# Performance work log

Hardware: AMD Instinct MI355X
Metric: run time of the kernel (lower is better)

Reference implementation:

```python
import jax, jax.numpy as jnp
import numpy as np

B, W, T, D = 64, 32, 4096, 128

def setup_inputs() -> dict:
    key = jax.random.key(0)
    ks = jax.random.split(key, 10)
    s = 1.0 / np.sqrt(D)
    return {
        "x": jax.random.normal(ks[0], (B, W, T), dtype=jnp.float32),
        "enc_w": jax.random.uniform(ks[1], (D, W), jnp.float32, -1/np.sqrt(W), 1/np.sqrt(W)),
        "enc_b": jax.random.uniform(ks[2], (D,), jnp.float32, -1/np.sqrt(W), 1/np.sqrt(W)),
        "w_ih": jax.random.uniform(ks[3], (3 * D, D), jnp.float32, -s, s),
        "w_hh": jax.random.uniform(ks[4], (3 * D, D), jnp.float32, -s, s),
        "b_ih": jax.random.uniform(ks[5], (3 * D,), jnp.float32, -s, s),
        "b_hh": jax.random.uniform(ks[6], (3 * D,), jnp.float32, -s, s),
        "dec_w": jax.random.uniform(ks[7], (1, D), jnp.float32, -s, s),
        "dec_b": jax.random.uniform(ks[8], (1,), jnp.float32, -s, s),
        "scale": jnp.ones((1,), dtype=jnp.float32),
        "noise_eps": jax.random.normal(ks[9], (B, T), dtype=jnp.float32),
    }

def reference(x, enc_w, enc_b, w_ih, w_hh, b_ih, b_hh, dec_w, dec_b, scale, noise_eps):
    # x: [B, W, T] -> src: [T, B, W]
    src = jnp.transpose(x, (2, 0, 1))
    encoded = src @ enc_w.T + enc_b  # [T, B, D] (dropout is identity at inference)

    def gru_step(h, xt):
        gi = xt @ w_ih.T + b_ih  # [B, 3D]
        gh = h @ w_hh.T + b_hh   # [B, 3D]
        i_r, i_z, i_n = jnp.split(gi, 3, axis=-1)
        h_r, h_z, h_n = jnp.split(gh, 3, axis=-1)
        r = jax.nn.sigmoid(i_r + h_r)
        z = jax.nn.sigmoid(i_z + h_z)
        n = jnp.tanh(i_n + r * h_n)
        h_new = (1.0 - z) * n + z * h
        return h_new, h_new

    h0 = jnp.zeros_like(encoded[0])
    _, res = jax.lax.scan(gru_step, h0, encoded)  # res: [T, B, D]

    out = encoded + res
    out = (out @ dec_w.T + dec_b)[..., 0]  # [T, B]
    out = out.T                            # [B, T]
    noise = scale * noise_eps              # scale * randn_like(x[:, -1, :])
    return jax.nn.relu(out + noise)
```

## Files before the change

kernel.cpp:

```cpp
#include <hip/hip_runtime.h>

#define NB 64
#define NW 32
#define NT 4096
#define ND 128

typedef __attribute__((ext_vector_type(8))) short short8;
typedef __attribute__((ext_vector_type(4))) float f32x4;

#define BAR_LGKM() asm volatile("s_waitcnt lgkmcnt(0)\n\ts_barrier" ::: "memory")

static __device__ __forceinline__ float sigm_f(float v) {
    float e = __builtin_amdgcn_exp2f(v * -1.4426950408889634f);
    return __builtin_amdgcn_rcpf(1.0f + e);
}
static __device__ __forceinline__ float tanh_f(float v) {
    float e = __builtin_amdgcn_exp2f(v * 2.8853900817779268f);
    return 1.0f - 2.0f * __builtin_amdgcn_rcpf(1.0f + e);
}
static __device__ __forceinline__ unsigned short f2bf(float f) {
    unsigned u = __float_as_uint(f);
    u += 0x7FFFu + ((u >> 16) & 1u);
    return (unsigned short)(u >> 16);
}

__global__ __launch_bounds__(256) void k_xv(
    const float* __restrict__ x, const float* __restrict__ enc_w,
    const float* __restrict__ enc_b, const float* __restrict__ dec_w,
    const float* __restrict__ dec_b, const float* __restrict__ scale,
    const float* __restrict__ noise, float* __restrict__ out)
{
    __shared__ float v_s[NW];
    __shared__ float c2_s;
    const int tid = threadIdx.x;
    if (tid < NW) {
        float s = 0.0f;
        for (int d = 0; d < ND; ++d) s = fmaf(enc_w[d * NW + tid], dec_w[d], s);
        v_s[tid] = s;
    } else if (tid == 64) {
        float s = 0.0f;
        for (int d = 0; d < ND; ++d) s = fmaf(enc_b[d], dec_w[d], s);
        c2_s = s + dec_b[0];
    }
    __syncthreads();
    const int flat = blockIdx.x * 256 + tid;
    const int b = flat >> 12;
    const int t = flat & (NT - 1);
    float acc = c2_s + scale[0] * noise[flat];
    const float* xr = x + (size_t)b * NW * NT + t;
    #pragma unroll
    for (int w = 0; w < NW; ++w) acc = fmaf(xr[(size_t)w * NT], v_s[w], acc);
    out[flat] = acc;
}

__global__ __launch_bounds__(512, 2) void k_gru(
    const float* __restrict__ x, const float* __restrict__ enc_w,
    const float* __restrict__ enc_b, const float* __restrict__ w_ih,
    const float* __restrict__ w_hh, const float* __restrict__ b_ih,
    const float* __restrict__ b_hh, const float* __restrict__ dec_w,
    float* out)
{
    __shared__ float encw_s[ND * NW];
    __shared__ float encb_s[ND];
    __shared__ alignas(16) unsigned short h_lds[2][ND];
    __shared__ alignas(16) unsigned short x_s[2][32][NW];
    __shared__ alignas(16) float xv_lds[NT];
    __shared__ alignas(16) float out_lds[NT];

    const int tid  = threadIdx.x;
    const int b    = blockIdx.x;
    const int wv   = tid >> 6;
    const int lane = tid & 63;
    const int g    = lane >> 4;
    const int c    = lane & 15;
    const int d    = wv * 16 + c;

    const size_t xbase = (size_t)b * NW * NT;
    float* outb = out + (size_t)b * NT;

    for (int i = tid; i < ND * NW; i += 512) encw_s[i] = enc_w[i];
    if (tid < ND) { encb_s[tid] = enc_b[tid]; h_lds[0][tid] = 0; h_lds[1][tid] = 0; }
    if (tid < 256) {
        int w = tid >> 3, tc = (tid & 7) * 4;
        float4 v = *(const float4*)&x[xbase + (size_t)w * NT + tc];
        x_s[0][tc+0][w] = f2bf(v.x);
        x_s[0][tc+1][w] = f2bf(v.y);
        x_s[0][tc+2][w] = f2bf(v.z);
        x_s[0][tc+3][w] = f2bf(v.w);
    }
    for (int i = tid; i < NT / 4; i += 512)
        ((float4*)xv_lds)[i] = ((const float4*)outb)[i];
    __syncthreads();

    short8 BR[4], BZ[4], BN[4];
    #pragma unroll
    for (int kt = 0; kt < 4; ++kt) {
        const float* pr = w_hh + (size_t)(0*ND + d) * ND + kt*32 + g*8;
        const float* pz = w_hh + (size_t)(1*ND + d) * ND + kt*32 + g*8;
        const float* pn = w_hh + (size_t)(2*ND + d) * ND + kt*32 + g*8;
        #pragma unroll
        for (int i = 0; i < 8; ++i) {
            BR[kt][i] = (short)f2bf(pr[i]);
            BZ[kt][i] = (short)f2bf(pz[i]);
            BN[kt][i] = (short)f2bf(pn[i]);
        }
    }

    short8 BD[4];
    #pragma unroll
    for (int kt = 0; kt < 4; ++kt)
        #pragma unroll
        for (int i = 0; i < 8; ++i)
            BD[kt][i] = (short)f2bf(dec_w[kt*32 + g*8 + i]);

    short8 XR, XZ, XN;
    {
        const float* rr = w_ih + (size_t)(0*ND + d) * ND;
        const float* rz = w_ih + (size_t)(1*ND + d) * ND;
        const float* rn = w_ih + (size_t)(2*ND + d) * ND;
        #pragma unroll
        for (int i = 0; i < 8; ++i) {
            int w = g*8 + i;
            float ar = 0.0f, az = 0.0f, an = 0.0f;
            for (int dp = 0; dp < ND; ++dp) {
                float ew = encw_s[dp*NW + w];
                ar = fmaf(ew, rr[dp], ar);
                az = fmaf(ew, rz[dp], az);
                an = fmaf(ew, rn[dp], an);
            }
            XR[i] = (short)f2bf(ar); XZ[i] = (short)f2bf(az); XN[i] = (short)f2bf(an);
        }
    }

    float cR, cZ, cGN, cIN;
    {
        const float* rr = w_ih + (size_t)(0*ND + d) * ND;
        const float* rz = w_ih + (size_t)(1*ND + d) * ND;
        const float* rn = w_ih + (size_t)(2*ND + d) * ND;
        float b0 = b_ih[d], b1 = b_ih[ND+d], b2 = b_ih[2*ND+d];
        for (int dp = 0; dp < ND; ++dp) {
            float eb = encb_s[dp];
            b0 = fmaf(eb, rr[dp], b0);
            b1 = fmaf(eb, rz[dp], b1);
            b2 = fmaf(eb, rn[dp], b2);
        }
        cR  = b0 + b_hh[d];
        cZ  = b1 + b_hh[ND+d];
        cGN = b_hh[2*ND+d];
        cIN = b2;
    }
    const f32x4 cRv  = {cR, cR, cR, cR};
    const f32x4 cZv  = {cZ, cZ, cZ, cZ};
    const f32x4 cGNv = {cGN, cGN, cGN, cGN};
    const f32x4 cINv = {cIN, cIN, cIN, cIN};
    const f32x4 zv   = {0.f, 0.f, 0.f, 0.f};

    float h = 0.0f;
    float4 xpf = make_float4(0.f, 0.f, 0.f, 0.f);

    short8 XA_n = ((const short8*)x_s[0][0])[g];
    f32x4 aRx = __builtin_amdgcn_mfma_f32_16x16x32_bf16(XA_n, XR, cRv, 0, 0, 0);
    f32x4 aZx = __builtin_amdgcn_mfma_f32_16x16x32_bf16(XA_n, XZ, cZv, 0, 0, 0);
    f32x4 aIN = __builtin_amdgcn_mfma_f32_16x16x32_bf16(XA_n, XN, cINv, 0, 0, 0);

    #pragma unroll 1
    for (int t = 0; t < NT; ++t) {
        const int tl = t & 31;
        const int xb = (t >> 5) & 1;
        const int rb = t & 1;

        const short8* hp = (const short8*)h_lds[rb];
        short8 HA0 = hp[0*4 + g];
        short8 HA1 = hp[1*4 + g];
        short8 HA2 = hp[2*4 + g];
        short8 HA3 = hp[3*4 + g];
        {
            const int tn = (t + 1) & (NT - 1);
            XA_n = ((const short8*)x_s[(tn >> 5) & 1][tn & 31])[g];
        }

        f32x4 aR1 = __builtin_amdgcn_mfma_f32_16x16x32_bf16(HA0, BR[0], zv,  0, 0, 0);
        f32x4 aR2 = __builtin_amdgcn_mfma_f32_16x16x32_bf16(HA2, BR[2], aRx, 0, 0, 0);
        aR1 = __builtin_amdgcn_mfma_f32_16x16x32_bf16(HA1, BR[1], aR1, 0, 0, 0);
        aR2 = __builtin_amdgcn_mfma_f32_16x16x32_bf16(HA3, BR[3], aR2, 0, 0, 0);
        f32x4 aZ1 = __builtin_amdgcn_mfma_f32_16x16x32_bf16(HA0, BZ[0], zv,  0, 0, 0);
        f32x4 aZ2 = __builtin_amdgcn_mfma_f32_16x16x32_bf16(HA2, BZ[2], aZx, 0, 0, 0);
        aZ1 = __builtin_amdgcn_mfma_f32_16x16x32_bf16(HA1, BZ[1], aZ1, 0, 0, 0);
        aZ2 = __builtin_amdgcn_mfma_f32_16x16x32_bf16(HA3, BZ[3], aZ2, 0, 0, 0);
        f32x4 aN1 = __builtin_amdgcn_mfma_f32_16x16x32_bf16(HA0, BN[0], cGNv, 0, 0, 0);
        f32x4 aN2 = __builtin_amdgcn_mfma_f32_16x16x32_bf16(HA2, BN[2], zv,  0, 0, 0);
        aN1 = __builtin_amdgcn_mfma_f32_16x16x32_bf16(HA1, BN[1], aN1, 0, 0, 0);
        aN2 = __builtin_amdgcn_mfma_f32_16x16x32_bf16(HA3, BN[3], aN2, 0, 0, 0);

        if (t > 0 && wv == (t & 7)) {
            f32x4 aD1 = __builtin_amdgcn_mfma_f32_16x16x32_bf16(HA0, BD[0], zv, 0, 0, 0);
            f32x4 aD2 = __builtin_amdgcn_mfma_f32_16x16x32_bf16(HA2, BD[2], zv, 0, 0, 0);
            aD1 = __builtin_amdgcn_mfma_f32_16x16x32_bf16(HA1, BD[1], aD1, 0, 0, 0);
            aD2 = __builtin_amdgcn_mfma_f32_16x16x32_bf16(HA3, BD[3], aD2, 0, 0, 0);
            if (lane == 0) out_lds[t - 1] = aD1[0] + aD2[0];
        }

        if (tl == 0 && t + 32 < NT && tid < 256) {
            int w = tid >> 3, tc = (tid & 7) * 4;
            xpf = *(const float4*)&x[xbase + (size_t)w * NT + (t + 32) + tc];
        }
        if (tl == 16 && t + 16 < NT && tid < 256) {
            int w = tid >> 3, tc = (tid & 7) * 4;
            x_s[xb^1][tc+0][w] = f2bf(xpf.x);
            x_s[xb^1][tc+1][w] = f2bf(xpf.y);
            x_s[xb^1][tc+2][w] = f2bf(xpf.z);
            x_s[xb^1][tc+3][w] = f2bf(xpf.w);
        }

        f32x4 nRx = __builtin_amdgcn_mfma_f32_16x16x32_bf16(XA_n, XR, cRv, 0, 0, 0);
        f32x4 nZx = __builtin_amdgcn_mfma_f32_16x16x32_bf16(XA_n, XZ, cZv, 0, 0, 0);
        f32x4 nIN = __builtin_amdgcn_mfma_f32_16x16x32_bf16(XA_n, XN, cINv, 0, 0, 0);

        float R  = aR1[0] + aR2[0];
        float r_ = sigm_f(R);
        float Z  = aZ1[0] + aZ2[0];
        float z_ = sigm_f(Z);
        float GN = aN1[0] + aN2[0];
        float IN = aIN[0];
        float n_ = tanh_f(fmaf(r_, GN, IN));
        h = fmaf(z_, h - n_, n_);
        if (lane < 16) h_lds[rb ^ 1][d] = f2bf(h);

        aRx = nRx; aZx = nZx; aIN = nIN;
        BAR_LGKM();
    }

    if (wv == 0) {
        const short8* hp = (const short8*)h_lds[0];
        short8 HA0 = hp[0*4 + g];
        short8 HA1 = hp[1*4 + g];
        short8 HA2 = hp[2*4 + g];
        short8 HA3 = hp[3*4 + g];
        f32x4 aD1 = __builtin_amdgcn_mfma_f32_16x16x32_bf16(HA0, BD[0], zv, 0, 0, 0);
        f32x4 aD2 = __builtin_amdgcn_mfma_f32_16x16x32_bf16(HA2, BD[2], zv, 0, 0, 0);
        aD1 = __builtin_amdgcn_mfma_f32_16x16x32_bf16(HA1, BD[1], aD1, 0, 0, 0);
        aD2 = __builtin_amdgcn_mfma_f32_16x16x32_bf16(HA3, BD[3], aD2, 0, 0, 0);
        if (lane == 0) out_lds[NT - 1] = aD1[0] + aD2[0];
    }
    __syncthreads();
    for (int i = tid; i < NT / 4; i += 512) {
        float4 o = ((const float4*)out_lds)[i];
        float4 v = ((const float4*)xv_lds)[i];
        float4 r;
        r.x = fmaxf(o.x + v.x, 0.0f);
        r.y = fmaxf(o.y + v.y, 0.0f);
        r.z = fmaxf(o.z + v.z, 0.0f);
        r.w = fmaxf(o.w + v.w, 0.0f);
        ((float4*)outb)[i] = r;
    }
}

extern "C" void kernel_launch(void* const* d_in, const int* in_sizes, int n_in,
                              void* d_out, int out_size, void* d_ws, size_t ws_size,
                              hipStream_t stream) {
    const float* x      = (const float*)d_in[0];
    const float* enc_w  = (const float*)d_in[1];
    const float* enc_b  = (const float*)d_in[2];
    const float* w_ih   = (const float*)d_in[3];
    const float* w_hh   = (const float*)d_in[4];
    const float* b_ih   = (const float*)d_in[5];
    const float* b_hh   = (const float*)d_in[6];
    const float* dec_w  = (const float*)d_in[7];
    const float* dec_b  = (const float*)d_in[8];
    const float* scale  = (const float*)d_in[9];
    const float* noise  = (const float*)d_in[10];
    float* out = (float*)d_out;

    k_xv<<<(NB * NT) / 256, 256, 0, stream>>>(x, enc_w, enc_b, dec_w, dec_b, scale, noise, out);
    k_gru<<<NB, 512, 0, stream>>>(x, enc_w, enc_b, w_ih, w_hh, b_ih, b_hh, dec_w, out);
}
```

Baseline: 2.074 ms.

## Precompute input gates in 32-step chunks into LDS and batch decoder over h ring

Input-gate projections are now computed once per 32-step chunk with full MFMA row utilisation and stored in an LDS ring, so the serial loop only reads three floats instead of issuing three per-step MFMAs on the input. Hidden states are kept in a 32-entry LDS ring so the decoder projection can be done 16 timesteps at a time by one wave, replacing the per-step decoder MFMA. This cuts MFMA work on the critical per-step path. It costs more LDS (gi ring plus h ring) and adds periodic heavier steps when a chunk is refilled.

```diff
diff --git a/kernel.cpp b/kernel.cpp
--- a/kernel.cpp
+++ b/kernel.cpp
@@ -4,6 +4,9 @@
 #define NW 32
 #define NT 4096
 #define ND 128
+
+#define GI_STRIDE 388
+#define HR_STRIDE 144
 
 typedef __attribute__((ext_vector_type(8))) short short8;
 typedef __attribute__((ext_vector_type(4))) float f32x4;
@@ -60,10 +63,9 @@
     const float* __restrict__ b_hh, const float* __restrict__ dec_w,
     float* out)
 {
-    __shared__ float encw_s[ND * NW];
+    __shared__ alignas(16) float gi_lds[64 * GI_STRIDE];
     __shared__ float encb_s[ND];
-    __shared__ alignas(16) unsigned short h_lds[2][ND];
-    __shared__ alignas(16) unsigned short x_s[2][32][NW];
+    __shared__ alignas(16) unsigned short h_ring[32 * HR_STRIDE];
     __shared__ alignas(16) float xv_lds[NT];
     __shared__ alignas(16) float out_lds[NT];
 
@@ -77,17 +79,11 @@
 
     const size_t xbase = (size_t)b * NW * NT;
     float* outb = out + (size_t)b * NT;
+    float* encw_s = gi_lds;
 
     for (int i = tid; i < ND * NW; i += 512) encw_s[i] = enc_w[i];
-    if (tid < ND) { encb_s[tid] = enc_b[tid]; h_lds[0][tid] = 0; h_lds[1][tid] = 0; }
-    if (tid < 256) {
-        int w = tid >> 3, tc = (tid & 7) * 4;
-        float4 v = *(const float4*)&x[xbase + (size_t)w * NT + tc];
-        x_s[0][tc+0][w] = f2bf(v.x);
-        x_s[0][tc+1][w] = f2bf(v.y);
-        x_s[0][tc+2][w] = f2bf(v.z);
-        x_s[0][tc+3][w] = f2bf(v.w);
-    }
+    if (tid < ND) encb_s[tid] = enc_b[tid];
+    for (int i = tid; i < 32 * HR_STRIDE; i += 512) h_ring[i] = 0;
     for (int i = tid; i < NT / 4; i += 512)
         ((float4*)xv_lds)[i] = ((const float4*)outb)[i];
     __syncthreads();
@@ -155,36 +151,60 @@
     const f32x4 cINv = {cIN, cIN, cIN, cIN};
     const f32x4 zv   = {0.f, 0.f, 0.f, 0.f};
 
+    __syncthreads();
+
+    float xf[16];
+    #pragma unroll
+    for (int q = 0; q < 16; ++q)
+        xf[q] = x[xbase + (size_t)(g*8 + (q & 7)) * NT + ((q >> 3) * 16 + c)];
+    {
+        short8 xA0, xA1;
+        #pragma unroll
+        for (int i = 0; i < 8; ++i) { xA0[i] = (short)f2bf(xf[i]); xA1[i] = (short)f2bf(xf[8+i]); }
+        f32x4 gR0 = __builtin_amdgcn_mfma_f32_16x16x32_bf16(xA0, XR, cRv, 0, 0, 0);
+        f32x4 gR1 = __builtin_amdgcn_mfma_f32_16x16x32_bf16(xA1, XR, cRv, 0, 0, 0);
+        f32x4 gZ0 = __builtin_amdgcn_mfma_f32_16x16x32_bf16(xA0, XZ, cZv, 0, 0, 0);
+        f32x4 gZ1 = __builtin_amdgcn_mfma_f32_16x16x32_bf16(xA1, XZ, cZv, 0, 0, 0);
+        f32x4 gN0 = __builtin_amdgcn_mfma_f32_16x16x32_bf16(xA0, XN, cINv, 0, 0, 0);
+        f32x4 gN1 = __builtin_amdgcn_mfma_f32_16x16x32_bf16(xA1, XN, cINv, 0, 0, 0);
+        #pragma unroll
+        for (int r = 0; r < 4; ++r) {
+            int ti = 4*g + r;
+            gi_lds[(ti     )*GI_STRIDE +       d] = gR0[r];
+            gi_lds[(ti     )*GI_STRIDE + 128 + d] = gZ0[r];
+            gi_lds[(ti     )*GI_STRIDE + 256 + d] = gN0[r];
+            gi_lds[(ti + 16)*GI_STRIDE +       d] = gR1[r];
+            gi_lds[(ti + 16)*GI_STRIDE + 128 + d] = gZ1[r];
+            gi_lds[(ti + 16)*GI_STRIDE + 256 + d] = gN1[r];
+        }
+    }
+    #pragma unroll
+    for (int q = 0; q < 16; ++q)
+        xf[q] = x[xbase + (size_t)(g*8 + (q & 7)) * NT + (32 + (q >> 3) * 16 + c)];
+
+    __syncthreads();
+
     float h = 0.0f;
-    float4 xpf = make_float4(0.f, 0.f, 0.f, 0.f);
-
-    short8 XA_n = ((const short8*)x_s[0][0])[g];
-    f32x4 aRx = __builtin_amdgcn_mfma_f32_16x16x32_bf16(XA_n, XR, cRv, 0, 0, 0);
-    f32x4 aZx = __builtin_amdgcn_mfma_f32_16x16x32_bf16(XA_n, XZ, cZv, 0, 0, 0);
-    f32x4 aIN = __builtin_amdgcn_mfma_f32_16x16x32_bf16(XA_n, XN, cINv, 0, 0, 0);
 
     #pragma unroll 1
     for (int t = 0; t < NT; ++t) {
-        const int tl = t & 31;
-        const int xb = (t >> 5) & 1;
-        const int rb = t & 1;
-
-        const short8* hp = (const short8*)h_lds[rb];
-        short8 HA0 = hp[0*4 + g];
-        short8 HA1 = hp[1*4 + g];
-        short8 HA2 = hp[2*4 + g];
-        short8 HA3 = hp[3*4 + g];
-        {
-            const int tn = (t + 1) & (NT - 1);
-            XA_n = ((const short8*)x_s[(tn >> 5) & 1][tn & 31])[g];
-        }
+        const short8* hp = (const short8*)(h_ring + (size_t)((t + 31) & 31) * HR_STRIDE);
+        const short8 HA0 = hp[0*4 + g];
+        const short8 HA1 = hp[1*4 + g];
+        const short8 HA2 = hp[2*4 + g];
+        const short8 HA3 = hp[3*4 + g];
+
+        const float* gp = gi_lds + (size_t)(t & 63) * GI_STRIDE + d;
+        const float giR = gp[0];
+        const float giZ = gp[128];
+        const float giN = gp[256];
 
         f32x4 aR1 = __builtin_amdgcn_mfma_f32_16x16x32_bf16(HA0, BR[0], zv,  0, 0, 0);
-        f32x4 aR2 = __builtin_amdgcn_mfma_f32_16x16x32_bf16(HA2, BR[2], aRx, 0, 0, 0);
+        f32x4 aR2 = __builtin_amdgcn_mfma_f32_16x16x32_bf16(HA2, BR[2], zv,  0, 0, 0);
         aR1 = __builtin_amdgcn_mfma_f32_16x16x32_bf16(HA1, BR[1], aR1, 0, 0, 0);
         aR2 = __builtin_amdgcn_mfma_f32_16x16x32_bf16(HA3, BR[3], aR2, 0, 0, 0);
         f32x4 aZ1 = __builtin_amdgcn_mfma_f32_16x16x32_bf16(HA0, BZ[0], zv,  0, 0, 0);
-        f32x4 aZ2 = __builtin_amdgcn_mfma_f32_16x16x32_bf16(HA2, BZ[2], aZx, 0, 0, 0);
+        f32x4 aZ2 = __builtin_amdgcn_mfma_f32_16x16x32_bf16(HA2, BZ[2], zv,  0, 0, 0);
         aZ1 = __builtin_amdgcn_mfma_f32_16x16x32_bf16(HA1, BZ[1], aZ1, 0, 0, 0);
         aZ2 = __builtin_amdgcn_mfma_f32_16x16x32_bf16(HA3, BZ[3], aZ2, 0, 0, 0);
         f32x4 aN1 = __builtin_amdgcn_mfma_f32_16x16x32_bf16(HA0, BN[0], cGNv, 0, 0, 0);
@@ -192,55 +212,81 @@
         aN1 = __builtin_amdgcn_mfma_f32_16x16x32_bf16(HA1, BN[1], aN1, 0, 0, 0);
         aN2 = __builtin_amdgcn_mfma_f32_16x16x32_bf16(HA3, BN[3], aN2, 0, 0, 0);
 
-        if (t > 0 && wv == (t & 7)) {
-            f32x4 aD1 = __builtin_amdgcn_mfma_f32_16x16x32_bf16(HA0, BD[0], zv, 0, 0, 0);
-            f32x4 aD2 = __builtin_amdgcn_mfma_f32_16x16x32_bf16(HA2, BD[2], zv, 0, 0, 0);
-            aD1 = __builtin_amdgcn_mfma_f32_16x16x32_bf16(HA1, BD[1], aD1, 0, 0, 0);
-            aD2 = __builtin_amdgcn_mfma_f32_16x16x32_bf16(HA3, BD[3], aD2, 0, 0, 0);
-            if (lane == 0) out_lds[t - 1] = aD1[0] + aD2[0];
-        }
-
-        if (tl == 0 && t + 32 < NT && tid < 256) {
-            int w = tid >> 3, tc = (tid & 7) * 4;
-            xpf = *(const float4*)&x[xbase + (size_t)w * NT + (t + 32) + tc];
-        }
-        if (tl == 16 && t + 16 < NT && tid < 256) {
-            int w = tid >> 3, tc = (tid & 7) * 4;
-            x_s[xb^1][tc+0][w] = f2bf(xpf.x);
-            x_s[xb^1][tc+1][w] = f2bf(xpf.y);
-            x_s[xb^1][tc+2][w] = f2bf(xpf.z);
-            x_s[xb^1][tc+3][w] = f2bf(xpf.w);
-        }
-
-        f32x4 nRx = __builtin_amdgcn_mfma_f32_16x16x32_bf16(XA_n, XR, cRv, 0, 0, 0);
-        f32x4 nZx = __builtin_amdgcn_mfma_f32_16x16x32_bf16(XA_n, XZ, cZv, 0, 0, 0);
-        f32x4 nIN = __builtin_amdgcn_mfma_f32_16x16x32_bf16(XA_n, XN, cINv, 0, 0, 0);
-
-        float R  = aR1[0] + aR2[0];
+        if ((t & 31) == 8) {
+            const int t0n = (t & ~31) + 32;
+            if (t0n < NT) {
+                short8 xA0, xA1;
+                #pragma unroll
+                for (int i = 0; i < 8; ++i) { xA0[i] = (short)f2bf(xf[i]); xA1[i] = (short)f2bf(xf[8+i]); }
+                f32x4 gR0 = __builtin_amdgcn_mfma_f32_16x16x32_bf16(xA0, XR, cRv, 0, 0, 0);
+                f32x4 gR1 = __builtin_amdgcn_mfma_f32_16x16x32_bf16(xA1, XR, cRv, 0, 0, 0);
+                f32x4 gZ0 = __builtin_amdgcn_mfma_f32_16x16x32_bf16(xA0, XZ, cZv, 0, 0, 0);
+                f32x4 gZ1 = __builtin_amdgcn_mfma_f32_16x16x32_bf16(xA1, XZ, cZv, 0, 0, 0);
+                f32x4 gN0 = __builtin_amdgcn_mfma_f32_16x16x32_bf16(xA0, XN, cINv, 0, 0, 0);
+                f32x4 gN1 = __builtin_amdgcn_mfma_f32_16x16x32_bf16(xA1, XN, cINv, 0, 0, 0);
+                const int rbw = t0n & 63;
+                #pragma unroll
+                for (int r = 0; r < 4; ++r) {
+                    int ti = rbw + 4*g + r;
+                    gi_lds[(ti     )*GI_STRIDE +       d] = gR0[r];
+                    gi_lds[(ti     )*GI_STRIDE + 128 + d] = gZ0[r];
+                    gi_lds[(ti     )*GI_STRIDE + 256 + d] = gN0[r];
+                    gi_lds[(ti + 16)*GI_STRIDE +       d] = gR1[r];
+                    gi_lds[(ti + 16)*GI_STRIDE + 128 + d] = gZ1[r];
+                    gi_lds[(ti + 16)*GI_STRIDE + 256 + d] = gN1[r];
+                }
+                const int t0p = t0n + 32;
+                if (t0p < NT) {
+                    #pragma unroll
+                    for (int q = 0; q < 16; ++q)
+                        xf[q] = x[xbase + (size_t)(g*8 + (q & 7)) * NT + (t0p + (q >> 3) * 16 + c)];
+                }
+            }
+        }
+
+        if ((t & 15) == 0 && t >= 16 && wv == (((t >> 4) - 1) & 7)) {
+            const short8* hq = (const short8*)(h_ring + (size_t)(((t - 16) & 31) + c) * HR_STRIDE);
+            short8 AD0 = hq[0*4 + g];
+            short8 AD1 = hq[1*4 + g];
+            short8 AD2 = hq[2*4 + g];
+            short8 AD3 = hq[3*4 + g];
+            f32x4 aD1 = __builtin_amdgcn_mfma_f32_16x16x32_bf16(AD0, BD[0], zv, 0, 0, 0);
+            f32x4 aD2 = __builtin_amdgcn_mfma_f32_16x16x32_bf16(AD2, BD[2], zv, 0, 0, 0);
+            aD1 = __builtin_amdgcn_mfma_f32_16x16x32_bf16(AD1, BD[1], aD1, 0, 0, 0);
+            aD2 = __builtin_amdgcn_mfma_f32_16x16x32_bf16(AD3, BD[3], aD2, 0, 0, 0);
+            if (c == 0) {
+                #pragma unroll
+                for (int r = 0; r < 4; ++r)
+                    out_lds[(t - 16) + 4*g + r] = aD1[r] + aD2[r];
+            }
+        }
+
+        float R  = aR1[0] + aR2[0] + giR;
         float r_ = sigm_f(R);
-        float Z  = aZ1[0] + aZ2[0];
+        float Z  = aZ1[0] + aZ2[0] + giZ;
         float z_ = sigm_f(Z);
         float GN = aN1[0] + aN2[0];
-        float IN = aIN[0];
-        float n_ = tanh_f(fmaf(r_, GN, IN));
+        float n_ = tanh_f(fmaf(r_, GN, giN));
         h = fmaf(z_, h - n_, n_);
-        if (lane < 16) h_lds[rb ^ 1][d] = f2bf(h);
-
-        aRx = nRx; aZx = nZx; aIN = nIN;
+        if (lane < 16) h_ring[(size_t)(t & 31) * HR_STRIDE + d] = f2bf(h);
         BAR_LGKM();
     }
 
-    if (wv == 0) {
-        const short8* hp = (const short8*)h_lds[0];
-        short8 HA0 = hp[0*4 + g];
-        short8 HA1 = hp[1*4 + g];
-        short8 HA2 = hp[2*4 + g];
-        short8 HA3 = hp[3*4 + g];
-        f32x4 aD1 = __builtin_amdgcn_mfma_f32_16x16x32_bf16(HA0, BD[0], zv, 0, 0, 0);
-        f32x4 aD2 = __builtin_amdgcn_mfma_f32_16x16x32_bf16(HA2, BD[2], zv, 0, 0, 0);
-        aD1 = __builtin_amdgcn_mfma_f32_16x16x32_bf16(HA1, BD[1], aD1, 0, 0, 0);
-        aD2 = __builtin_amdgcn_mfma_f32_16x16x32_bf16(HA3, BD[3], aD2, 0, 0, 0);
-        if (lane == 0) out_lds[NT - 1] = aD1[0] + aD2[0];
+    if (wv == 7) {
+        const short8* hq = (const short8*)(h_ring + (size_t)(16 + c) * HR_STRIDE);
+        short8 AD0 = hq[0*4 + g];
+        short8 AD1 = hq[1*4 + g];
+        short8 AD2 = hq[2*4 + g];
+        short8 AD3 = hq[3*4 + g];
+        f32x4 aD1 = __builtin_amdgcn_mfma_f32_16x16x32_bf16(AD0, BD[0], zv, 0, 0, 0);
+        f32x4 aD2 = __builtin_amdgcn_mfma_f32_16x16x32_bf16(AD2, BD[2], zv, 0, 0, 0);
+        aD1 = __builtin_amdgcn_mfma_f32_16x16x32_bf16(AD1, BD[1], aD1, 0, 0, 0);
+        aD2 = __builtin_amdgcn_mfma_f32_16x16x32_bf16(AD3, BD[3], aD2, 0, 0, 0);
+        if (c == 0) {
+            #pragma unroll
+            for (int r = 0; r < 4; ++r)
+                out_lds[(NT - 16) + 4*g + r] = aD1[r] + aD2[r];
+        }
     }
     __syncthreads();
     for (int i = tid; i < NT / 4; i += 512) {
```

After: 1.801 ms. 13.2% less time.
